# Optimization experiments

Hardware: AMD Instinct MI355X
Metric: run time of the kernel (lower is better)

Reference implementation:

```python
import jax, jax.numpy as jnp
import numpy as np

B, C, L, D = 32, 1, 1024, 128


def _attention_matrix(x0, x1):
    # x0, x1: [B, 1, L, D]. A[b,0,i,j] = 1 / (1 + ||x0[b,0,i] - x1[b,0,j]||_2)
    a = x0[:, 0]  # [B, L, D]
    b = x1[:, 0]  # [B, L, D]
    # cdist via expansion: ||a_i - b_j||^2 = |a_i|^2 + |b_j|^2 - 2 a_i . b_j
    sq_a = jnp.sum(a * a, axis=-1)                      # [B, L]
    sq_b = jnp.sum(b * b, axis=-1)                      # [B, L]
    inner = jnp.einsum('bid,bjd->bij', a, b)            # [B, L, L]
    d2 = jnp.maximum(sq_a[:, :, None] + sq_b[:, None, :] - 2.0 * inner, 0.0)
    dist = jnp.sqrt(d2)
    A = 1.0 / (1.0 + dist)                              # [B, L, L]
    return A[:, None, :, :]                             # [B, 1, L, L]


def setup_inputs() -> dict:
    key = jax.random.key(0)
    k0, k1, kw0, kw1 = jax.random.split(key, 4)
    x0 = jax.random.normal(k0, (B, C, L, D), dtype=jnp.float32)
    x1 = jax.random.normal(k1, (B, C, L, D), dtype=jnp.float32)
    W0 = jax.random.normal(kw0, (L, D), dtype=jnp.float32)
    W1 = jax.random.normal(kw1, (L, D), dtype=jnp.float32)
    return {"x0": x0, "x1": x1, "W0": W0, "W1": W1}


def reference(x0, x1, W0, W1):
    A = _attention_matrix(x0, x1)                 # [B, 1, L, L]
    A_t = jnp.swapaxes(A, -1, -2)                 # [B, 1, L, L]
    a0 = jnp.matmul(A, W0)                        # [B, 1, L, D]
    a1 = jnp.matmul(A_t, W1)                      # [B, 1, L, D]
    f0 = jnp.concatenate([x0, a0], axis=1)        # [B, 2, L, D]
    f1 = jnp.concatenate([x1, a1], axis=1)        # [B, 2, L, D]
    return (f0, f1)
```

## Files before the change

### kernel.cpp

```cpp
#include <hip/hip_runtime.h>

#define B_ 32
#define L_ 1024
#define D_ 128
#define NT 512

typedef __attribute__((ext_vector_type(8))) short bf8_t;
typedef __attribute__((ext_vector_type(4))) float f4_t;

__device__ __forceinline__ unsigned cvtpk(float lo, float hi) {
  unsigned r;
  asm("v_cvt_pk_bf16_f32 %0, %1, %2" : "=v"(r) : "v"(lo), "v"(hi));
  return r;
}

__device__ __forceinline__ void gload16(const void* g, void* l) {
  __builtin_amdgcn_global_load_lds((const __attribute__((address_space(1))) void*)g,
                                   (__attribute__((address_space(3))) void*)l, 16, 0, 0);
}

__global__ __launch_bounds__(256)
void prep_kernel(const float* __restrict__ x0, const float* __restrict__ x1,
                 const float* __restrict__ W0, const float* __restrict__ W1,
                 short* __restrict__ Xs, float* __restrict__ sq,
                 short* __restrict__ Wt, float* __restrict__ out) {
  int bid = blockIdx.x;
  if (bid < 8192) {
    int t = bid * 256 + threadIdx.x;
    int row_id = t >> 5;
    int qp = t & 31;
    int which = row_id >> 15;
    int b = (row_id >> 10) & 31;
    int row = row_id & 1023;
    const float* x = which ? x1 : x0;
    float4 v = *(const float4*)(x + ((size_t)b * L_ + row) * D_ + qp * 4);
    float* o = out + (size_t)which * (B_ * 2 * L_ * D_) + (size_t)b * (2 * L_ * D_)
             + (size_t)row * D_ + qp * 4;
    *(float4*)o = v;
    unsigned w0 = cvtpk(v.x, v.y), w1 = cvtpk(v.z, v.w);
    char* xb = (char*)Xs + (size_t)row_id * 256 + ((qp * 8) ^ ((row & 7) << 4));
    *(uint2*)xb = make_uint2(w0, w1);
    float s = v.x * v.x + v.y * v.y + v.z * v.z + v.w * v.w;
    s += __shfl_xor(s, 1); s += __shfl_xor(s, 2); s += __shfl_xor(s, 4);
    s += __shfl_xor(s, 8); s += __shfl_xor(s, 16);
    if (qp == 0) sq[row_id] = s;
  } else {
    int idx = (bid - 8192) * 256 + threadIdx.x;
    int which = idx >> 17;
    int rm = idx & 131071;
    int j32 = rm >> 12;
    int d = (rm >> 5) & 127;
    int jj = rm & 31;
    const float* W = which ? W1 : W0;
    float wv = W[(j32 * 32 + jj) * D_ + d];
    Wt[idx] = (short)(cvtpk(wv, wv) & 0xffffu);
  }
}

__global__ __launch_bounds__(NT, 6)
void fused_attnconv(const short* __restrict__ Xs, const float* __restrict__ sq,
                    const short* __restrict__ Wt, float* __restrict__ out) {
  __shared__ char smem[36864];
  char* Pbase = smem + 16384;
  float* sqyL = (float*)(smem + 32768);

  const int bid = blockIdx.x;
  const int x = bid & 7, g = bid >> 3;
  const int p = x + 8 * (g >> 4);
  const int it = g & 15;
  const int which = p >> 5, b = p & 31;
  const int i0 = it * 64;
  const int po = (which ^ 1) * 32 + b;

  const char* apanel = (const char*)Xs + (size_t)p * (L_ * 256);
  const char* ypanel = (const char*)Xs + (size_t)po * (L_ * 256);
  const float* sqx_p = sq + p * L_;
  const float* sqy_p = sq + po * L_;
  float* Oc1 = out + (size_t)which * (B_ * 2 * L_ * D_) + (size_t)b * (2 * L_ * D_) + (L_ * D_);

  const int tid = threadIdx.x;
  const int lane = tid & 63;
  const int w = tid >> 6;
  const int l15 = lane & 15;
  const int q = lane >> 4;
  const int wr = w & 3;
  const int wc = w >> 2;
  const int I0 = wr * 16;
  const int JS = wc * 16;
  const int D0 = wc * 64;
  const int swz = (l15 & 7) << 4;

  bf8_t afr[4];
#pragma unroll
  for (int kb = 0; kb < 4; ++kb)
    afr[kb] = *(const bf8_t*)(apanel + (size_t)(i0 + I0 + l15) * 256 + ((kb * 64 + q * 16) ^ swz));
  const float sxv = sqx_p[i0 + I0 + l15];

  if (tid < 256) {
    *(f4_t*)(sqyL + tid * 4) = *(const f4_t*)(sqy_p + tid * 4);
  }
  gload16(ypanel + tid * 16, smem + tid * 16);

  f4_t z4 = {0.f, 0.f, 0.f, 0.f};
  f4_t acc[4] = {z4, z4, z4, z4};

  __syncthreads();

  for (int jt = 0; jt < 32; ++jt) {
    const int cur = jt & 1;
    char* yB = smem + cur * 8192;
    char* Pw = Pbase + cur * 8192;

    if (jt < 31)
      gload16(ypanel + (jt + 1) * 8192 + tid * 16, smem + (1 - cur) * 8192 + tid * 16);

    const short* Wb = Wt + which * 131072 + jt * 4096;
    bf8_t wf[4];
#pragma unroll
    for (int m = 0; m < 4; ++m)
      wf[m] = *(const bf8_t*)(Wb + (D0 + m * 16 + l15) * 32 + q * 8);

    f4_t sy = *(const f4_t*)(sqyL + jt * 32 + JS + q * 4);

    f4_t ST = z4;
#pragma unroll
    for (int kb = 0; kb < 4; ++kb) {
      const int kc = (kb * 64 + q * 16) ^ swz;
      bf8_t yf = *(const bf8_t*)(yB + (JS + l15) * 256 + kc);
      ST = __builtin_amdgcn_mfma_f32_16x16x32_bf16(yf, afr[kb], ST, 0, 0, 0);
    }

    {
      float A0 = __builtin_amdgcn_rcpf(1.0f + __builtin_amdgcn_sqrtf(fmaxf(__builtin_fmaf(-2.f, ST[0], sxv + sy[0]), 0.f)));
      float A1 = __builtin_amdgcn_rcpf(1.0f + __builtin_amdgcn_sqrtf(fmaxf(__builtin_fmaf(-2.f, ST[1], sxv + sy[1]), 0.f)));
      float A2 = __builtin_amdgcn_rcpf(1.0f + __builtin_amdgcn_sqrtf(fmaxf(__builtin_fmaf(-2.f, ST[2], sxv + sy[2]), 0.f)));
      float A3 = __builtin_amdgcn_rcpf(1.0f + __builtin_amdgcn_sqrtf(fmaxf(__builtin_fmaf(-2.f, ST[3], sxv + sy[3]), 0.f)));
      *(uint2*)(Pw + (I0 + l15) * 128 + ((JS * 2 + q * 8) ^ swz)) =
          make_uint2(cvtpk(A0, A1), cvtpk(A2, A3));
    }

    __syncthreads();

    bf8_t pf = *(const bf8_t*)(Pw + (I0 + l15) * 128 + ((q * 16) ^ swz));
#pragma unroll
    for (int m = 0; m < 4; ++m)
      acc[m] = __builtin_amdgcn_mfma_f32_16x16x32_bf16(pf, wf[m], acc[m], 0, 0, 0);
  }

#pragma unroll
  for (int m = 0; m < 4; ++m) {
    const int d = D0 + m * 16 + l15;
#pragma unroll
    for (int r = 0; r < 4; ++r)
      Oc1[(size_t)(i0 + I0 + q * 4 + r) * D_ + d] = acc[m][r];
  }
}

extern "C" void kernel_launch(void* const* d_in, const int* in_sizes, int n_in,
                              void* d_out, int out_size, void* d_ws, size_t ws_size,
                              hipStream_t stream) {
  const float* x0 = (const float*)d_in[0];
  const float* x1 = (const float*)d_in[1];
  const float* W0 = (const float*)d_in[2];
  const float* W1 = (const float*)d_in[3];
  float* out = (float*)d_out;

  char* ws = (char*)d_ws;
  short* Wt = (short*)ws;
  short* Xs = (short*)(ws + 524288);
  float* sq = (float*)(ws + 524288 + 16777216);

  prep_kernel<<<9216, 256, 0, stream>>>(x0, x1, W0, W1, Xs, sq, Wt, out);
  fused_attnconv<<<1024, NT, 0, stream>>>(Xs, sq, Wt, out);
}
```

Measured before the change: 103.6 us.

## Feed attention tile to second MFMA from registers, drop LDS round trip

The bf16 attention fragment now goes straight from registers into the second MFMA as a K=32 operand with its upper half zero-padded. This removes the LDS store, barrier and reload of P, and W is repacked in prep so its fragment layout matches. Each wave now covers all 128 output columns over its own 16-column slice of j, and the two wave partners sum their partial accumulators through LDS at the end. In exchange the second-stage MFMA count doubles because half of each K is zeros, register pressure rises (occupancy hint lowered from 6 to 4), and the W buffer doubles in size.

```diff
diff --git a/kernel.cpp b/kernel.cpp
--- a/kernel.cpp
+++ b/kernel.cpp
@@ -46,22 +46,31 @@
     if (qp == 0) sq[row_id] = s;
   } else {
     int idx = (bid - 8192) * 256 + threadIdx.x;
-    int which = idx >> 17;
-    int rm = idx & 131071;
-    int j32 = rm >> 12;
-    int d = (rm >> 5) & 127;
-    int jj = rm & 31;
-    const float* W = which ? W1 : W0;
-    float wv = W[(j32 * 32 + jj) * D_ + d];
-    Wt[idx] = (short)(cvtpk(wv, wv) & 0xffffu);
+    int which = idx >> 18;
+    int rm = idx & 262143;
+    int frag = rm >> 9;
+    int s9 = rm & 511;
+    int lane = s9 >> 3;
+    int e = s9 & 7;
+    int m = frag & 7;
+    int wc = (frag >> 3) & 1;
+    int jt = frag >> 4;
+    short val = 0;
+    if (e < 4) {
+      const float* W = which ? W1 : W0;
+      int j = jt * 32 + wc * 16 + (lane >> 4) * 4 + e;
+      int d = m * 16 + (lane & 15);
+      float wv = W[j * D_ + d];
+      val = (short)(cvtpk(wv, wv) & 0xffffu);
+    }
+    Wt[idx] = val;
   }
 }
 
-__global__ __launch_bounds__(NT, 6)
+__global__ __launch_bounds__(NT, 4)
 void fused_attnconv(const short* __restrict__ Xs, const float* __restrict__ sq,
                     const short* __restrict__ Wt, float* __restrict__ out) {
   __shared__ char smem[36864];
-  char* Pbase = smem + 16384;
   float* sqyL = (float*)(smem + 32768);
 
   const int bid = blockIdx.x;
@@ -87,7 +96,6 @@
   const int wc = w >> 2;
   const int I0 = wr * 16;
   const int JS = wc * 16;
-  const int D0 = wc * 64;
   const int swz = (l15 & 7) << 4;
 
   bf8_t afr[4];
@@ -102,23 +110,24 @@
   gload16(ypanel + tid * 16, smem + tid * 16);
 
   f4_t z4 = {0.f, 0.f, 0.f, 0.f};
-  f4_t acc[4] = {z4, z4, z4, z4};
+  f4_t acc[8];
+#pragma unroll
+  for (int m = 0; m < 8; ++m) acc[m] = z4;
 
   __syncthreads();
 
   for (int jt = 0; jt < 32; ++jt) {
     const int cur = jt & 1;
     char* yB = smem + cur * 8192;
-    char* Pw = Pbase + cur * 8192;
 
     if (jt < 31)
       gload16(ypanel + (jt + 1) * 8192 + tid * 16, smem + (1 - cur) * 8192 + tid * 16);
 
-    const short* Wb = Wt + which * 131072 + jt * 4096;
-    bf8_t wf[4];
+    const short* Wb = Wt + which * 262144 + ((jt * 2 + wc) * 8) * 512 + lane * 8;
+    bf8_t wf[8];
 #pragma unroll
-    for (int m = 0; m < 4; ++m)
-      wf[m] = *(const bf8_t*)(Wb + (D0 + m * 16 + l15) * 32 + q * 8);
+    for (int m = 0; m < 8; ++m)
+      wf[m] = *(const bf8_t*)(Wb + m * 512);
 
     f4_t sy = *(const f4_t*)(sqyL + jt * 32 + JS + q * 4);
 
@@ -130,29 +139,35 @@
       ST = __builtin_amdgcn_mfma_f32_16x16x32_bf16(yf, afr[kb], ST, 0, 0, 0);
     }
 
-    {
-      float A0 = __builtin_amdgcn_rcpf(1.0f + __builtin_amdgcn_sqrtf(fmaxf(__builtin_fmaf(-2.f, ST[0], sxv + sy[0]), 0.f)));
-      float A1 = __builtin_amdgcn_rcpf(1.0f + __builtin_amdgcn_sqrtf(fmaxf(__builtin_fmaf(-2.f, ST[1], sxv + sy[1]), 0.f)));
-      float A2 = __builtin_amdgcn_rcpf(1.0f + __builtin_amdgcn_sqrtf(fmaxf(__builtin_fmaf(-2.f, ST[2], sxv + sy[2]), 0.f)));
-      float A3 = __builtin_amdgcn_rcpf(1.0f + __builtin_amdgcn_sqrtf(fmaxf(__builtin_fmaf(-2.f, ST[3], sxv + sy[3]), 0.f)));
-      *(uint2*)(Pw + (I0 + l15) * 128 + ((JS * 2 + q * 8) ^ swz)) =
-          make_uint2(cvtpk(A0, A1), cvtpk(A2, A3));
-    }
+    float A0 = __builtin_amdgcn_rcpf(1.0f + __builtin_amdgcn_sqrtf(fmaxf(__builtin_fmaf(-2.f, ST[0], sxv + sy[0]), 0.f)));
+    float A1 = __builtin_amdgcn_rcpf(1.0f + __builtin_amdgcn_sqrtf(fmaxf(__builtin_fmaf(-2.f, ST[1], sxv + sy[1]), 0.f)));
+    float A2 = __builtin_amdgcn_rcpf(1.0f + __builtin_amdgcn_sqrtf(fmaxf(__builtin_fmaf(-2.f, ST[2], sxv + sy[2]), 0.f)));
+    float A3 = __builtin_amdgcn_rcpf(1.0f + __builtin_amdgcn_sqrtf(fmaxf(__builtin_fmaf(-2.f, ST[3], sxv + sy[3]), 0.f)));
+    union { int4 i4; bf8_t s8; } pu;
+    pu.i4 = make_int4((int)cvtpk(A0, A1), (int)cvtpk(A2, A3), 0, 0);
+    bf8_t pf = pu.s8;
+
+#pragma unroll
+    for (int m = 0; m < 8; ++m)
+      acc[m] = __builtin_amdgcn_mfma_f32_16x16x32_bf16(pf, wf[m], acc[m], 0, 0, 0);
 
     __syncthreads();
-
-    bf8_t pf = *(const bf8_t*)(Pw + (I0 + l15) * 128 + ((q * 16) ^ swz));
-#pragma unroll
-    for (int m = 0; m < 4; ++m)
-      acc[m] = __builtin_amdgcn_mfma_f32_16x16x32_bf16(pf, wf[m], acc[m], 0, 0, 0);
   }
 
+  f4_t* ex = (f4_t*)smem;
+  const int partner = w ^ 4;
 #pragma unroll
-  for (int m = 0; m < 4; ++m) {
-    const int d = D0 + m * 16 + l15;
+  for (int k = 0; k < 4; ++k)
+    ex[w * 256 + k * 64 + lane] = acc[(1 - wc) * 4 + k];
+  __syncthreads();
+#pragma unroll
+  for (int k = 0; k < 4; ++k) {
+    const int m = wc * 4 + k;
+    f4_t other = ex[partner * 256 + k * 64 + lane];
+    const int d = m * 16 + l15;
 #pragma unroll
     for (int r = 0; r < 4; ++r)
-      Oc1[(size_t)(i0 + I0 + q * 4 + r) * D_ + d] = acc[m][r];
+      Oc1[(size_t)(i0 + I0 + q * 4 + r) * D_ + d] = acc[m][r] + other[r];
   }
 }
 
@@ -167,9 +182,9 @@
 
   char* ws = (char*)d_ws;
   short* Wt = (short*)ws;
-  short* Xs = (short*)(ws + 524288);
-  float* sq = (float*)(ws + 524288 + 16777216);
+  short* Xs = (short*)(ws + 1048576);
+  float* sq = (float*)(ws + 1048576 + 16777216);
 
-  prep_kernel<<<9216, 256, 0, stream>>>(x0, x1, W0, W1, Xs, sq, Wt, out);
+  prep_kernel<<<10240, 256, 0, stream>>>(x0, x1, W0, W1, Xs, sq, Wt, out);
   fused_attnconv<<<1024, NT, 0, stream>>>(Xs, sq, Wt, out);
 }
```

Result: slower. 120.8 us (+16.6%).
